# Kernel tuning notes

Measured on AMD Instinct MI355X. Metric: run time of the kernel, lower is better.

The kernel has to match this reference:

```python
import jax, jax.numpy as jnp
import numpy as np

# DeepSpeed FixedSparsityConfig defaults (attention='unidirectional')
BLOCK = 16
NUM_LOCAL_BLOCKS = 4   # local window = 4 blocks = 64 tokens
D_MODEL = 1024
N_HEADS = 16
HEAD_DIM = D_MODEL // N_HEADS


def _block_layout(seq_len: int) -> np.ndarray:
    """Token-level boolean mask [S,S] from the fixed unidirectional block layout.
    Allowed iff: (same 4-block local window AND block_k <= block_q) OR
                 (block_k % 4 == 3 AND block_k <= block_q)  (causal global column).
    Same layout for every head (different_layout_per_head=False)."""
    nb = seq_len // BLOCK
    r = np.arange(nb)
    causal = r[None, :] <= r[:, None]
    same_win = (r[:, None] // NUM_LOCAL_BLOCKS) == (r[None, :] // NUM_LOCAL_BLOCKS)
    glob = (r[None, :] % NUM_LOCAL_BLOCKS) == (NUM_LOCAL_BLOCKS - 1)
    layout = (same_win & causal) | (glob & causal)
    return np.kron(layout, np.ones((BLOCK, BLOCK), dtype=bool))


def setup_inputs() -> dict:
    key = jax.random.key(0)
    ks = jax.random.split(key, 7)
    B, S = 2, 2048
    init = 1.0 / np.sqrt(D_MODEL)
    x = jax.random.normal(ks[0], (B, S, D_MODEL), jnp.float32)
    key_padding_mask = jnp.zeros((B, S), jnp.float32)  # additive mask ('add' mode)
    Wq = jax.random.normal(ks[1], (D_MODEL, D_MODEL), jnp.float32) * init
    Wk = jax.random.normal(ks[2], (D_MODEL, D_MODEL), jnp.float32) * init
    Wv = jax.random.normal(ks[3], (D_MODEL, D_MODEL), jnp.float32) * init
    bq = jax.random.normal(ks[4], (D_MODEL,), jnp.float32) * 0.01
    bk = jax.random.normal(ks[5], (D_MODEL,), jnp.float32) * 0.01
    bv = jax.random.normal(ks[6], (D_MODEL,), jnp.float32) * 0.01
    return dict(x=x, key_padding_mask=key_padding_mask,
                Wq=Wq, bq=bq, Wk=Wk, bk=bk, Wv=Wv, bv=bv)


def reference(x, key_padding_mask, Wq, bq, Wk, bk, Wv, bv):
    B, S, D = x.shape
    q = (x @ Wq + bq).reshape(B, S, N_HEADS, HEAD_DIM)
    k = (x @ Wk + bk).reshape(B, S, N_HEADS, HEAD_DIM)
    v = (x @ Wv + bv).reshape(B, S, N_HEADS, HEAD_DIM)
    scale = HEAD_DIM ** -0.5  # DeepSpeed scales by head_size**-0.5 inside softmax
    scores = jnp.einsum('bqhd,bkhd->bhqk', q, k) * scale
    scores = scores + key_padding_mask[:, None, None, :]
    mask = jnp.asarray(_block_layout(S))  # [S,S] bool; absent blocks excluded from softmax
    scores = jnp.where(mask[None, None], scores, -jnp.inf)
    attn = jax.nn.softmax(scores, axis=-1)
    out = jnp.einsum('bhqk,bkhd->bqhd', attn, v)
    return out.reshape(B, S, D)
```

## Files before the change

kernel.cpp:

```cpp
#include <hip/hip_runtime.h>
#include <hip/hip_bf16.h>

typedef __bf16 bf16;
typedef __bf16 bf16x4 __attribute__((ext_vector_type(4)));
typedef __bf16 bf16x8 __attribute__((ext_vector_type(8)));
typedef float  f32x4  __attribute__((ext_vector_type(4)));

#define D_MODEL 1024
#define S_LEN   2048
#define BATCH   2
#define NH      16
#define HD      64
#define NX ((size_t)BATCH * S_LEN * D_MODEL)

__device__ inline void gl_lds16(const bf16* g, bf16* l) {
    __builtin_amdgcn_global_load_lds(
        (const __attribute__((address_space(1))) void*)g,
        (__attribute__((address_space(3))) void*)l, 16, 0, 0);
}

__global__ __launch_bounds__(256) void prep(
    const float* __restrict__ x, bf16* __restrict__ xb,
    const float* __restrict__ Wq, const float* __restrict__ Wk,
    const float* __restrict__ Wv, bf16* __restrict__ Wt)
{
    __shared__ bf16 tile[64 * 72];

    if (blockIdx.x < 2048) {
        const size_t base = ((size_t)blockIdx.x * 256 + threadIdx.x) * 8;
        const float4 a = *(const float4*)(x + base);
        const float4 b = *(const float4*)(x + base + 4);
        bf16x8 o;
        o[0] = (bf16)a.x; o[1] = (bf16)a.y; o[2] = (bf16)a.z; o[3] = (bf16)a.w;
        o[4] = (bf16)b.x; o[5] = (bf16)b.y; o[6] = (bf16)b.z; o[7] = (bf16)b.w;
        *(bf16x8*)(xb + base) = o;
        return;
    }

    const int id2 = blockIdx.x - 2048;
    const int z = id2 >> 8;
    const float* W = (z == 0) ? Wq : (z == 1) ? Wk : Wv;
    const int k0 = ((id2 >> 4) & 15) * 64, n0 = (id2 & 15) * 64;

    const int r16 = threadIdx.x >> 4, c4 = (threadIdx.x & 15) << 2;

#pragma unroll
    for (int rr = 0; rr < 4; ++rr) {
        const int row = rr * 16 + r16;
        const float4 v = *(const float4*)(W + (size_t)(k0 + row) * D_MODEL + n0 + c4);
        bf16x4 o; o[0] = (bf16)v.x; o[1] = (bf16)v.y; o[2] = (bf16)v.z; o[3] = (bf16)v.w;
        *(bf16x4*)(tile + row * 72 + c4) = o;
    }
    __syncthreads();
#pragma unroll
    for (int rr = 0; rr < 4; ++rr) {
        const int row = rr * 16 + r16;
        bf16x4 o;
#pragma unroll
        for (int j = 0; j < 4; ++j) o[j] = tile[(c4 + j) * 72 + row];
        *(bf16x4*)(Wt + (size_t)(z * D_MODEL + n0 + row) * D_MODEL + k0 + c4) = o;
    }
}

#define GNT 32

__device__ __forceinline__ void stage_A(
    const bf16* __restrict__ Xb, bf16* __restrict__ sA,
    int m0, int k0, int tid, int wave)
{
    const int ci0 = tid;
    const int r0 = ci0 >> 2, c0 = (ci0 & 3) ^ ((ci0 >> 3) & 3);
    gl_lds16(Xb + (size_t)(m0 + r0) * D_MODEL + k0 + c0 * 8, sA + wave * 512);
    const int ci1 = 512 + tid;
    const int r1 = ci1 >> 2, c1 = (ci1 & 3) ^ ((ci1 >> 3) & 3);
    gl_lds16(Xb + (size_t)(m0 + r1) * D_MODEL + k0 + c1 * 8, sA + 4096 + wave * 512);
}

__device__ __forceinline__ void stage_B(
    const bf16* __restrict__ Wt, bf16* __restrict__ sB,
    int n0, int k0, int tid, int wave, int lane)
{
    const int ci0 = tid;
    const int r0 = ci0 >> 2, c0 = (ci0 & 3) ^ ((ci0 >> 3) & 3);
    gl_lds16(Wt + (size_t)(n0 + r0) * D_MODEL + k0 + c0 * 8, sB + wave * 512);
    const int ci1 = 512 + wave * 32 + lane;
    const int r1 = ci1 >> 2, c1 = (ci1 & 3) ^ ((ci1 >> 3) & 3);
    if (lane < 32)
        gl_lds16(Wt + (size_t)(n0 + r1) * D_MODEL + k0 + c1 * 8, sB + 4096 + wave * 256);
}

template<int VM>
__device__ __forceinline__ void gemm_tile_body(
    const bf16* __restrict__ Xb, const bf16* __restrict__ Wt,
    bf16* __restrict__ As, bf16* __restrict__ Bs,
    int m0, int n0, int t, int tid, int wave, int lane, int wm, int wn,
    int col, int pchunk, f32x4 (&acc)[4][6])
{
    if constexpr (VM == 8)      asm volatile("s_waitcnt vmcnt(8)" ::: "memory");
    else if constexpr (VM == 4) asm volatile("s_waitcnt vmcnt(4)" ::: "memory");
    else                        asm volatile("s_waitcnt vmcnt(0)" ::: "memory");
    asm volatile("s_barrier" ::: "memory");

    const bf16* bufA = As + (t & 3) * 8192;
    const bf16* bufB = Bs + (t & 3) * 6144;
    const bool pf = (t + 3 < GNT);
    const int k3 = (t + 3) * 32;

    if (pf) stage_A(Xb, As + ((t + 3) & 3) * 8192, m0, k3, tid, wave);

    bf16x8 a[4], b[6];
#pragma unroll
    for (int mr = 0; mr < 4; ++mr)
        a[mr] = *(const bf16x8*)(bufA + (wm * 64 + mr * 16 + col) * 32 + pchunk * 8);
#pragma unroll
    for (int nr = 0; nr < 3; ++nr)
        b[nr] = *(const bf16x8*)(bufB + (wn * 96 + nr * 16 + col) * 32 + pchunk * 8);

    __builtin_amdgcn_s_setprio(1);
#pragma unroll
    for (int mr = 0; mr < 4; ++mr)
#pragma unroll
        for (int nr = 0; nr < 3; ++nr)
            acc[mr][nr] = __builtin_amdgcn_mfma_f32_16x16x32_bf16(a[mr], b[nr], acc[mr][nr], 0, 0, 0);
    __builtin_amdgcn_s_setprio(0);

    asm volatile("s_barrier" ::: "memory");
    if (pf) stage_B(Wt, Bs + ((t + 3) & 3) * 6144, n0, k3, tid, wave, lane);
#pragma unroll
    for (int nr = 3; nr < 6; ++nr)
        b[nr] = *(const bf16x8*)(bufB + (wn * 96 + nr * 16 + col) * 32 + pchunk * 8);

    __builtin_amdgcn_s_setprio(1);
#pragma unroll
    for (int mr = 0; mr < 4; ++mr)
#pragma unroll
        for (int nr = 3; nr < 6; ++nr)
            acc[mr][nr] = __builtin_amdgcn_mfma_f32_16x16x32_bf16(a[mr], b[nr], acc[mr][nr], 0, 0, 0);
    __builtin_amdgcn_s_setprio(0);
}

__global__ __launch_bounds__(512, 2) void gemm_qkv_dp(
    const bf16* __restrict__ Xb, const bf16* __restrict__ Wt,
    const float* __restrict__ bq, const float* __restrict__ bk,
    const float* __restrict__ bv, bf16* __restrict__ QKV)
{
    extern __shared__ bf16 smem[];
    bf16* As = smem;
    bf16* Bs = smem + 32768;

    const int bid = blockIdx.x, k = bid & 7, j = bid >> 3;
    const int nx = ((k >> 2) << 3) + (j & 7);
    const int my = ((k & 3) << 2) + (j >> 3);
    const int n0 = nx * 192, m0 = my * 256;

    const int tid = threadIdx.x, wave = tid >> 6, lane = tid & 63;
    const int wm = wave >> 1, wn = wave & 1;
    const int col = lane & 15, quad = lane >> 4;
    const int pchunk = quad ^ ((col >> 1) & 3);

    f32x4 acc[4][6] = {};

    stage_A(Xb, As,         m0,  0, tid, wave);  stage_B(Wt, Bs,         n0,  0, tid, wave, lane);
    stage_A(Xb, As + 8192,  m0, 32, tid, wave);  stage_B(Wt, Bs + 6144,  n0, 32, tid, wave, lane);
    stage_A(Xb, As + 16384, m0, 64, tid, wave);  stage_B(Wt, Bs + 12288, n0, 64, tid, wave, lane);

    for (int t = 0; t < GNT - 2; ++t)
        gemm_tile_body<8>(Xb, Wt, As, Bs, m0, n0, t, tid, wave, lane, wm, wn, col, pchunk, acc);
    gemm_tile_body<4>(Xb, Wt, As, Bs, m0, n0, GNT - 2, tid, wave, lane, wm, wn, col, pchunk, acc);
    gemm_tile_body<0>(Xb, Wt, As, Bs, m0, n0, GNT - 1, tid, wave, lane, wm, wn, col, pchunk, acc);

#pragma unroll
    for (int nr = 0; nr < 6; ++nr) {
        const int cg = n0 + wn * 96 + nr * 16 + col;
        const int z = cg >> 10, c = cg & 1023;
        const float bsv = (z == 0 ? bq : (z == 1 ? bk : bv))[c];
        const float scale = (z == 0) ? 0.125f : 1.0f;
        bf16* C = QKV + (size_t)z * NX;
#pragma unroll
        for (int mr = 0; mr < 4; ++mr)
#pragma unroll
            for (int i = 0; i < 4; ++i) {
                const int rg = m0 + wm * 64 + mr * 16 + quad * 4 + i;
                C[(size_t)rg * D_MODEL + c] = (bf16)((acc[mr][nr][i] + bsv) * scale);
            }
    }
}

__global__ __launch_bounds__(256, 4) void sparse_attn64(
    const bf16* __restrict__ Q, const bf16* __restrict__ Kv,
    const bf16* __restrict__ Vv, const float* __restrict__ kpm,
    float* __restrict__ out)
{
    const int lid = blockIdx.x + 32 * (blockIdx.y + 16 * blockIdx.z);
    const int xk = lid & 7, j = lid >> 3;
    const int pair = xk * 4 + (j & 3);
    const int h = pair & 15, b = pair >> 4;
    const int w = 31 - (j >> 2);

    const int t = threadIdx.x, wavei = t >> 6, lane = t & 63;
    const int col = lane & 15, quad = lane >> 4;
    const int qb = 4 * w + wavei;

    __shared__ bf16 KbS[64 * 72];
    __shared__ bf16 VtS[2][64 * 72];
    __shared__ bf16 Ps[4][16 * 72];

    const size_t qrow = ((size_t)(b * S_LEN + qb * 16 + col)) * D_MODEL + h * HD;
    const bf16x8 aq0 = *(const bf16x8*)(Q + qrow + quad * 8);
    const bf16x8 aq1 = *(const bf16x8*)(Q + qrow + 32 + quad * 8);

    f32x4 o[4] = {};
    float lacc[4] = {0.f, 0.f, 0.f, 0.f};

    const int nGlob = (w + 3) >> 2;
    const int niter = nGlob + 1;

    const int srow = t >> 2, sd16 = (t & 3) << 4;
    const int sg = srow >> 4, sr = srow & 15;
    const int p2 = t & 31, dg8 = (t >> 5) << 3;
    const int key0 = 2 * p2, vg = key0 >> 4, vr = key0 & 15;

    auto kb_of = [&](int it, int g) -> int {
        if (it >= nGlob) return 4 * w + g;
        const int jj = 4 * it + g;
        return (jj < w) ? (4 * jj + 3) : 3;
    };

    bf16x8 rk0, rk1, rv0, rv1;
    {
        const size_t krow = ((size_t)(b * S_LEN + kb_of(0, sg) * 16 + sr)) * D_MODEL + h * HD + sd16;
        rk0 = *(const bf16x8*)(Kv + krow);
        rk1 = *(const bf16x8*)(Kv + krow + 8);
        const size_t vrow = ((size_t)(b * S_LEN + kb_of(0, vg) * 16 + vr)) * D_MODEL + h * HD + dg8;
        rv0 = *(const bf16x8*)(Vv + vrow);
        rv1 = *(const bf16x8*)(Vv + vrow + D_MODEL);
        *(bf16x8*)(KbS + srow * 72 + sd16)     = rk0;
        *(bf16x8*)(KbS + srow * 72 + sd16 + 8) = rk1;
#pragma unroll
        for (int jj = 0; jj < 8; ++jj) {
            bf16 pr[2] = { rv0[jj], rv1[jj] };
            *(unsigned int*)(VtS[0] + (dg8 + jj) * 72 + key0) = *(unsigned int*)pr;
        }
    }

    for (int it = 0; it < niter; ++it) {
        __syncthreads();
        const int cur = it & 1, nxt = cur ^ 1;
        const bool more = (it + 1 < niter);
        if (more) {
            const size_t krow = ((size_t)(b * S_LEN + kb_of(it + 1, sg) * 16 + sr)) * D_MODEL + h * HD + sd16;
            rk0 = *(const bf16x8*)(Kv + krow);
            rk1 = *(const bf16x8*)(Kv + krow + 8);
            const size_t vrow = ((size_t)(b * S_LEN + kb_of(it + 1, vg) * 16 + vr)) * D_MODEL + h * HD + dg8;
            rv0 = *(const bf16x8*)(Vv + vrow);
            rv1 = *(const bf16x8*)(Vv + vrow + D_MODEL);
        }

        f32x4 s[4];
        float mval[4];
        bool  val[4];
#pragma unroll
        for (int g = 0; g < 4; ++g) {
            val[g] = (it == nGlob) ? (g <= wavei) : (4 * it + g < w);
            if (val[g]) {
                const int kb = kb_of(it, g);
                mval[g] = kpm[b * S_LEN + kb * 16 + col];
                f32x4 z = {};
                const bf16x8 bk0 = *(const bf16x8*)(KbS + (g * 16 + col) * 72 + quad * 8);
                const bf16x8 bk1 = *(const bf16x8*)(KbS + (g * 16 + col) * 72 + 32 + quad * 8);
                __builtin_amdgcn_s_setprio(1);
                z = __builtin_amdgcn_mfma_f32_16x16x32_bf16(aq0, bk0, z, 0, 0, 0);
                s[g] = __builtin_amdgcn_mfma_f32_16x16x32_bf16(aq1, bk1, z, 0, 0, 0);
                __builtin_amdgcn_s_setprio(0);
            }
        }

        __syncthreads();
        if (more) {
            *(bf16x8*)(KbS + srow * 72 + sd16)     = rk0;
            *(bf16x8*)(KbS + srow * 72 + sd16 + 8) = rk1;
        }

#pragma unroll
        for (int g = 0; g < 4; ++g) {
            if (val[g]) {
#pragma unroll
                for (int i = 0; i < 4; ++i) {
                    const float pv = __expf(s[g][i] + mval[g]);
                    lacc[i] += pv;
                    Ps[wavei][(quad * 4 + i) * 72 + g * 16 + col] = (bf16)pv;
                }
            } else {
#pragma unroll
                for (int i = 0; i < 4; ++i)
                    Ps[wavei][(quad * 4 + i) * 72 + g * 16 + col] = (bf16)0.0f;
            }
        }

        const bf16* Vt = VtS[cur];
        const bf16x8 aP0 = *(const bf16x8*)(Ps[wavei] + col * 72 + quad * 8);
        const bf16x8 aP1 = *(const bf16x8*)(Ps[wavei] + col * 72 + 32 + quad * 8);
        __builtin_amdgcn_s_setprio(1);
#pragma unroll
        for (int nt = 0; nt < 4; ++nt) {
            const bf16x8 b0 = *(const bf16x8*)(Vt + (nt * 16 + col) * 72 + quad * 8);
            const bf16x8 b1 = *(const bf16x8*)(Vt + (nt * 16 + col) * 72 + 32 + quad * 8);
            o[nt] = __builtin_amdgcn_mfma_f32_16x16x32_bf16(aP0, b0, o[nt], 0, 0, 0);
            o[nt] = __builtin_amdgcn_mfma_f32_16x16x32_bf16(aP1, b1, o[nt], 0, 0, 0);
        }
        __builtin_amdgcn_s_setprio(0);

        if (more) {
#pragma unroll
            for (int jj = 0; jj < 8; ++jj) {
                bf16 pr[2] = { rv0[jj], rv1[jj] };
                *(unsigned int*)(VtS[nxt] + (dg8 + jj) * 72 + key0) = *(unsigned int*)pr;
            }
        }
    }

#pragma unroll
    for (int i = 0; i < 4; ++i) {
        float rs = lacc[i];
        rs += __shfl_xor(rs, 1);
        rs += __shfl_xor(rs, 2);
        rs += __shfl_xor(rs, 4);
        rs += __shfl_xor(rs, 8);
        const float inv = 1.0f / rs;
        const int rg = b * S_LEN + qb * 16 + quad * 4 + i;
#pragma unroll
        for (int nt = 0; nt < 4; ++nt)
            out[(size_t)rg * D_MODEL + h * HD + nt * 16 + col] = o[nt][i] * inv;
    }
}

extern "C" void kernel_launch(void* const* d_in, const int* in_sizes, int n_in,
                              void* d_out, int out_size, void* d_ws, size_t ws_size,
                              hipStream_t stream)
{
    const float* x = nullptr; const float* kpm = nullptr;
    const float* Wp[3] = {nullptr, nullptr, nullptr};
    const float* bp[3] = {nullptr, nullptr, nullptr};
    int wn = 0, bn = 0;
    for (int i = 0; i < n_in; ++i) {
        const float* p = (const float*)d_in[i];
        const long s = in_sizes[i];
        if (s == (long)NX)            x = p;
        else if (s == BATCH * S_LEN)  kpm = p;
        else if (s == D_MODEL * D_MODEL && wn < 3) Wp[wn++] = p;
        else if (s == D_MODEL && bn < 3)           bp[bn++] = p;
    }

    bf16* Qb = (bf16*)d_ws;
    bf16* Kb = Qb + NX;
    bf16* Vb = Kb + NX;
    bf16* Xb = (bf16*)d_out;
    bf16* Wt = Xb + NX;
    float* outp = (float*)d_out;

    static bool attr_done = false;
    if (!attr_done) {
        (void)hipFuncSetAttribute(reinterpret_cast<const void*>(gemm_qkv_dp),
                                  hipFuncAttributeMaxDynamicSharedMemorySize, 114688);
        attr_done = true;
    }

    prep<<<2816, 256, 0, stream>>>(x, Xb, Wp[0], Wp[1], Wp[2], Wt);

    gemm_qkv_dp<<<dim3(256), 512, 114688, stream>>>(
        Xb, Wt, bp[0], bp[1], bp[2], Qb);

    sparse_attn64<<<dim3(S_LEN / 64, NH, BATCH), 256, 0, stream>>>(
        Qb, Kb, Vb, kpm, outp);
}
```

Baseline: 135.5 us.

## Halve QKV GEMM tile to 128x192 with 256-thread blocks and 512 blocks

The QKV projection GEMM moves from 256x192 tiles with 8 waves per block to 128x192 tiles with 4 waves, and launches twice as many blocks. The staging loops, LDS buffer offsets, vmcnt wait counts, block-index swizzle and the dynamic shared memory size are all rewritten to match the new load counts. The intent is better occupancy and CU load balance, since 512 blocks spread more evenly over the CUs and each block uses less LDS. In exchange, the B (weight) tile is reused across fewer rows, so global and L2 traffic for weights goes up.

```diff
diff --git a/kernel.cpp b/kernel.cpp
--- a/kernel.cpp
+++ b/kernel.cpp
@@ -71,42 +71,41 @@
     const int ci0 = tid;
     const int r0 = ci0 >> 2, c0 = (ci0 & 3) ^ ((ci0 >> 3) & 3);
     gl_lds16(Xb + (size_t)(m0 + r0) * D_MODEL + k0 + c0 * 8, sA + wave * 512);
-    const int ci1 = 512 + tid;
+    const int ci1 = 256 + tid;
     const int r1 = ci1 >> 2, c1 = (ci1 & 3) ^ ((ci1 >> 3) & 3);
-    gl_lds16(Xb + (size_t)(m0 + r1) * D_MODEL + k0 + c1 * 8, sA + 4096 + wave * 512);
+    gl_lds16(Xb + (size_t)(m0 + r1) * D_MODEL + k0 + c1 * 8, sA + 2048 + wave * 512);
 }
 
 __device__ __forceinline__ void stage_B(
     const bf16* __restrict__ Wt, bf16* __restrict__ sB,
-    int n0, int k0, int tid, int wave, int lane)
-{
-    const int ci0 = tid;
-    const int r0 = ci0 >> 2, c0 = (ci0 & 3) ^ ((ci0 >> 3) & 3);
-    gl_lds16(Wt + (size_t)(n0 + r0) * D_MODEL + k0 + c0 * 8, sB + wave * 512);
-    const int ci1 = 512 + wave * 32 + lane;
-    const int r1 = ci1 >> 2, c1 = (ci1 & 3) ^ ((ci1 >> 3) & 3);
-    if (lane < 32)
-        gl_lds16(Wt + (size_t)(n0 + r1) * D_MODEL + k0 + c1 * 8, sB + 4096 + wave * 256);
+    int n0, int k0, int tid, int wave)
+{
+#pragma unroll
+    for (int p = 0; p < 3; ++p) {
+        const int ci = p * 256 + tid;
+        const int r = ci >> 2, c = (ci & 3) ^ ((ci >> 3) & 3);
+        gl_lds16(Wt + (size_t)(n0 + r) * D_MODEL + k0 + c * 8, sB + p * 2048 + wave * 512);
+    }
 }
 
 template<int VM>
 __device__ __forceinline__ void gemm_tile_body(
     const bf16* __restrict__ Xb, const bf16* __restrict__ Wt,
     bf16* __restrict__ As, bf16* __restrict__ Bs,
-    int m0, int n0, int t, int tid, int wave, int lane, int wm, int wn,
+    int m0, int n0, int t, int tid, int wave, int wm, int wn,
     int col, int pchunk, f32x4 (&acc)[4][6])
 {
-    if constexpr (VM == 8)      asm volatile("s_waitcnt vmcnt(8)" ::: "memory");
-    else if constexpr (VM == 4) asm volatile("s_waitcnt vmcnt(4)" ::: "memory");
+    if constexpr (VM == 10)     asm volatile("s_waitcnt vmcnt(10)" ::: "memory");
+    else if constexpr (VM == 5) asm volatile("s_waitcnt vmcnt(5)" ::: "memory");
     else                        asm volatile("s_waitcnt vmcnt(0)" ::: "memory");
     asm volatile("s_barrier" ::: "memory");
 
-    const bf16* bufA = As + (t & 3) * 8192;
+    const bf16* bufA = As + (t & 3) * 4096;
     const bf16* bufB = Bs + (t & 3) * 6144;
     const bool pf = (t + 3 < GNT);
     const int k3 = (t + 3) * 32;
 
-    if (pf) stage_A(Xb, As + ((t + 3) & 3) * 8192, m0, k3, tid, wave);
+    if (pf) stage_A(Xb, As + ((t + 3) & 3) * 4096, m0, k3, tid, wave);
 
     bf16x8 a[4], b[6];
 #pragma unroll
@@ -125,7 +124,7 @@
     __builtin_amdgcn_s_setprio(0);
 
     asm volatile("s_barrier" ::: "memory");
-    if (pf) stage_B(Wt, Bs + ((t + 3) & 3) * 6144, n0, k3, tid, wave, lane);
+    if (pf) stage_B(Wt, Bs + ((t + 3) & 3) * 6144, n0, k3, tid, wave);
 #pragma unroll
     for (int nr = 3; nr < 6; ++nr)
         b[nr] = *(const bf16x8*)(bufB + (wn * 96 + nr * 16 + col) * 32 + pchunk * 8);
@@ -139,19 +138,19 @@
     __builtin_amdgcn_s_setprio(0);
 }
 
-__global__ __launch_bounds__(512, 2) void gemm_qkv_dp(
+__global__ __launch_bounds__(256, 2) void gemm_qkv_dp(
     const bf16* __restrict__ Xb, const bf16* __restrict__ Wt,
     const float* __restrict__ bq, const float* __restrict__ bk,
     const float* __restrict__ bv, bf16* __restrict__ QKV)
 {
     extern __shared__ bf16 smem[];
     bf16* As = smem;
-    bf16* Bs = smem + 32768;
+    bf16* Bs = smem + 16384;
 
     const int bid = blockIdx.x, k = bid & 7, j = bid >> 3;
-    const int nx = ((k >> 2) << 3) + (j & 7);
-    const int my = ((k & 3) << 2) + (j >> 3);
-    const int n0 = nx * 192, m0 = my * 256;
+    const int my = ((k & 3) << 3) + (j & 7);
+    const int nx = ((k >> 2) << 3) + (j >> 3);
+    const int m0 = my * 128, n0 = nx * 192;
 
     const int tid = threadIdx.x, wave = tid >> 6, lane = tid & 63;
     const int wm = wave >> 1, wn = wave & 1;
@@ -160,14 +159,14 @@
 
     f32x4 acc[4][6] = {};
 
-    stage_A(Xb, As,         m0,  0, tid, wave);  stage_B(Wt, Bs,         n0,  0, tid, wave, lane);
-    stage_A(Xb, As + 8192,  m0, 32, tid, wave);  stage_B(Wt, Bs + 6144,  n0, 32, tid, wave, lane);
-    stage_A(Xb, As + 16384, m0, 64, tid, wave);  stage_B(Wt, Bs + 12288, n0, 64, tid, wave, lane);
+    stage_A(Xb, As,         m0,  0, tid, wave);  stage_B(Wt, Bs,         n0,  0, tid, wave);
+    stage_A(Xb, As + 4096,  m0, 32, tid, wave);  stage_B(Wt, Bs + 6144,  n0, 32, tid, wave);
+    stage_A(Xb, As + 8192,  m0, 64, tid, wave);  stage_B(Wt, Bs + 12288, n0, 64, tid, wave);
 
     for (int t = 0; t < GNT - 2; ++t)
-        gemm_tile_body<8>(Xb, Wt, As, Bs, m0, n0, t, tid, wave, lane, wm, wn, col, pchunk, acc);
-    gemm_tile_body<4>(Xb, Wt, As, Bs, m0, n0, GNT - 2, tid, wave, lane, wm, wn, col, pchunk, acc);
-    gemm_tile_body<0>(Xb, Wt, As, Bs, m0, n0, GNT - 1, tid, wave, lane, wm, wn, col, pchunk, acc);
+        gemm_tile_body<10>(Xb, Wt, As, Bs, m0, n0, t, tid, wave, wm, wn, col, pchunk, acc);
+    gemm_tile_body<5>(Xb, Wt, As, Bs, m0, n0, GNT - 2, tid, wave, wm, wn, col, pchunk, acc);
+    gemm_tile_body<0>(Xb, Wt, As, Bs, m0, n0, GNT - 1, tid, wave, wm, wn, col, pchunk, acc);
 
 #pragma unroll
     for (int nr = 0; nr < 6; ++nr) {
@@ -361,13 +360,13 @@
     static bool attr_done = false;
     if (!attr_done) {
         (void)hipFuncSetAttribute(reinterpret_cast<const void*>(gemm_qkv_dp),
-                                  hipFuncAttributeMaxDynamicSharedMemorySize, 114688);
+                                  hipFuncAttributeMaxDynamicSharedMemorySize, 81920);
         attr_done = true;
     }
 
     prep<<<2816, 256, 0, stream>>>(x, Xb, Wp[0], Wp[1], Wp[2], Wt);
 
-    gemm_qkv_dp<<<dim3(256), 512, 114688, stream>>>(
+    gemm_qkv_dp<<<dim3(512), 256, 81920, stream>>>(
         Xb, Wt, bp[0], bp[1], bp[2], Qb);
 
     sparse_attn64<<<dim3(S_LEN / 64, NH, BATCH), 256, 0, stream>>>(
```

After: 137.0 us. About the same (+1.1%).
